# Kernel tuning notes

Hardware: AMD Instinct MI355X
Metric: run time of the kernel (lower is better)

The kernel has to match this reference:

```python
import jax, jax.numpy as jnp
import numpy as np
from jax import lax

B, S, C_IN, D, H, P, W, DFF, K = 32, 4096, 32, 256, 8, 24, 64, 512, 5
DH = D // H
EPS = 1e-5


def _make_starts():
    stride = max(1, W // 2)
    idx = list(range(0, max(S - W + 1, 1), stride))
    if len(idx) == 0 or idx[-1] != S - W:
        if S - W >= 0:
            idx.append(S - W)
    return np.asarray(idx)

STARTS = _make_starts()                      # [M]
WIDX = STARTS[:, None] + np.arange(W)        # [M, W] patch gather indices


def setup_inputs() -> dict:
    key = jax.random.key(0)
    ks = jax.random.split(key, 24)
    r = lambda i, shape, s=0.02: (jax.random.normal(ks[i], shape, jnp.float32) * s)
    return {
        "x": jax.random.normal(ks[0], (B, S, C_IN), jnp.float32),
        "last_close_unused": jnp.zeros((B,), jnp.float32),
        "dw_w": r(1, (C_IN, 1, K), 0.2),      # depthwise conv kernel
        "pw_w": r(2, (D, C_IN), 0.1),         # pointwise conv (1x1)
        "bn_g": jnp.ones((D,), jnp.float32),
        "bn_b": jnp.zeros((D,), jnp.float32),
        "lg_Wq": r(3, (D, D)), "lg_Wk": r(4, (D, D)),
        "lg_Wv": r(5, (D, D)), "lg_Wo": r(6, (D, D)),
        "dec_Qd": r(7, (P, D), 1.0 / np.sqrt(D)),
        "dec_Wq": r(8, (D, D)), "dec_Wk": r(9, (D, D)),
        "dec_Wv": r(10, (D, D)), "dec_Wo": r(11, (D, D)),
        "ff1_w": r(12, (DFF, D)), "ff1_b": jnp.zeros((DFF,), jnp.float32),
        "ff2_w": r(13, (D, DFF)), "ff2_b": jnp.zeros((D,), jnp.float32),
        "out_w": r(14, (1, D)), "out_b": jnp.zeros((1,), jnp.float32),
        "gate_logits": jnp.tile(jnp.array([0.2, 0.4, 0.4], jnp.float32), (P, 1)),
    }


def _ln(x):
    m = x.mean(-1, keepdims=True)
    v = ((x - m) ** 2).mean(-1, keepdims=True)
    return (x - m) / jnp.sqrt(v + EPS)


def _split(t):  # [B, L, D] -> [B, H, L, DH]
    return t.reshape(t.shape[0], -1, H, DH).transpose(0, 2, 1, 3)


def _mha(Q, KV, Wq, Wk, Wv, scale):
    q = _split(Q @ Wq.T)
    k = _split(KV @ Wk.T)
    v = _split(KV @ Wv.T)
    attn = jax.nn.softmax(jnp.einsum('bhqd,bhkd->bhqk', q, k) * scale, axis=-1)
    o = jnp.einsum('bhqk,bhkd->bhqd', attn, v)
    o = o.transpose(0, 2, 1, 3).reshape(Q.shape[0], -1, D)
    return o, attn


def reference(x, last_close_unused, dw_w, pw_w, bn_g, bn_b,
              lg_Wq, lg_Wk, lg_Wv, lg_Wo,
              dec_Qd, dec_Wq, dec_Wk, dec_Wv, dec_Wo,
              ff1_w, ff1_b, ff2_w, ff2_b, out_w, out_b, gate_logits):
    # --- DepthwisePointwise front-end ---
    xt = jnp.transpose(x, (0, 2, 1))                         # [B, C, S]
    z = lax.conv_general_dilated(xt, dw_w, (1,), [(K // 2, K // 2)],
                                 dimension_numbers=('NCH', 'OIH', 'NCH'),
                                 feature_group_count=C_IN)
    z = jnp.einsum('dc,bcs->bds', pw_w, z)                   # pointwise 1x1
    z = jax.nn.gelu(z, approximate=False)
    m = z.mean((0, 2), keepdims=True)                        # BatchNorm1d (batch stats)
    v = ((z - m) ** 2).mean((0, 2), keepdims=True)
    z = (z - m) / jnp.sqrt(v + EPS) * bn_g[None, :, None] + bn_b[None, :, None]
    z = jnp.transpose(z, (0, 2, 1))                          # [B, S, D]

    # --- LocalGlobalAttention: patch-mean queries over full sequence K/V ---
    Q = z[:, WIDX].mean(axis=2)                              # [B, M, D]
    scale = 1.0 / np.sqrt(DH)
    o, attn_g = _mha(Q, z, lg_Wq, lg_Wk, lg_Wv, scale)
    Hh = _ln(o @ lg_Wo.T + Q)                                # [B, M, D]

    # --- CrossDecoder: learned queries ---
    Qd = jnp.broadcast_to(dec_Qd[None], (B, P, D))
    o2, attn_d = _mha(Qd, Hh, dec_Wq, dec_Wk, dec_Wv, scale)
    z2 = _ln(o2 @ dec_Wo.T + Qd)
    u = jax.nn.gelu(z2 @ ff1_w.T + ff1_b, approximate=False)
    u = _ln(u @ ff2_w.T + ff2_b + z2)
    y_global = (u @ out_w.T + out_b)[..., 0]                 # [B, P]

    # --- Gated combine: residual=0, local=global ---
    g = jax.nn.softmax(gate_logits, axis=-1)                 # [P, 3]
    y = g[:, 1][None, :] * y_global + g[:, 2][None, :] * y_global
    return (y, attn_g, attn_d)
```

## Files before the change

### kernel.cpp

```cpp
#include <hip/hip_runtime.h>
#include <hip/hip_bf16.h>
#include <cmath>

typedef unsigned short u16;
typedef __attribute__((ext_vector_type(4))) float f32x4;
typedef __attribute__((ext_vector_type(8))) short s16x8;

__device__ __forceinline__ float b2f(u16 u) { return __uint_as_float(((unsigned)u) << 16); }
__device__ __forceinline__ u16 f2b(float f) {
    unsigned u = __float_as_uint(f);
    unsigned r = (u + 0x7fffu + ((u >> 16) & 1u)) >> 16;
    return (u16)r;
}
__device__ __forceinline__ float gelu_f(float x) {
    float t = x * (0.7978845608f + 0.0356774081f * x * x);
    float e = exp2f(2.885390082f * t);
    return 0.5f * x * (1.0f + (e - 1.0f) / (e + 1.0f));
}

#define FOLD 0.25503590f

__global__ __launch_bounds__(256) void prep0_k(const float* __restrict__ pw_w,
        const float* __restrict__ lg_Wq, const float* __restrict__ lg_Wo,
        const float* __restrict__ dec_Wk, const float* __restrict__ dec_Wv,
        const float* __restrict__ dec_Wo, const float* __restrict__ ff1_w,
        const float* __restrict__ ff2_w,
        u16* __restrict__ pwb, u16* __restrict__ Wq_b, u16* __restrict__ Wo_b,
        u16* __restrict__ Wk2_b, u16* __restrict__ Wv2_b, u16* __restrict__ Wo2b,
        u16* __restrict__ ff1b, u16* __restrict__ ff2b)
{
    int idx = blockIdx.x * 256 + threadIdx.x;
    if (idx < 327680) {
        int which = idx >> 16, r = idx & 65535;
        const float* srcs[5] = {lg_Wq, lg_Wo, dec_Wk, dec_Wv, dec_Wo};
        u16* dsts[5] = {Wq_b, Wo_b, Wk2_b, Wv2_b, Wo2b};
        dsts[which][r] = f2b(srcs[which][r]);
    } else if (idx < 458752) {
        int r = idx - 327680;
        ff1b[r] = f2b(ff1_w[r]);
    } else if (idx < 589824) {
        int r = idx - 458752;
        ff2b[r] = f2b(ff2_w[r]);
    } else {
        int r = idx - 589824;
        pwb[r] = f2b(pw_w[r]);
    }
}

__global__ __launch_bounds__(256) void dwpw_k(const float* __restrict__ x,
        const float* __restrict__ dw_w, const u16* __restrict__ pwb,
        u16* __restrict__ zp, float* __restrict__ csum, float* __restrict__ csum2)
{
    __shared__ float xs[68][33];
    __shared__ __align__(16) u16 As[64][40];
    const int t = threadIdx.x;
    const int b = blockIdx.x >> 6, s0 = (blockIdx.x & 63) << 6;
    const int r0 = blockIdx.x * 64;
    const int lane = t & 63, w = t >> 6;
    const int l16 = lane & 15, hi = lane >> 4;

    for (int idx = t; idx < 68 * 32; idx += 256) {
        int row = idx >> 5, c = idx & 31;
        int sg = s0 - 2 + row;
        xs[row][c] = (sg >= 0 && sg < 4096) ? x[((size_t)b * 4096 + sg) * 32 + c] : 0.0f;
    }
    const int cc = t & 31;
    float wv[5];
    #pragma unroll
    for (int k = 0; k < 5; ++k) wv[k] = dw_w[cc * 5 + k];
    __syncthreads();
    #pragma unroll
    for (int i = 0; i < 8; ++i) {
        int sl = (t + i * 256) >> 5;
        float acc = 0;
        #pragma unroll
        for (int k = 0; k < 5; ++k) acc += xs[sl + k][cc] * wv[k];
        As[sl][cc] = f2b(acc);
    }
    __syncthreads();

    const int n0 = w * 64;
    f32x4 zero = {0, 0, 0, 0};
    s16x8 bf[4];
    #pragma unroll
    for (int ni = 0; ni < 4; ++ni)
        bf[ni] = *(const s16x8*)(pwb + (n0 + ni * 16 + l16) * 32 + hi * 8);

    float cl[4] = {0,0,0,0}, ch[4] = {0,0,0,0};
    float ql[4] = {0,0,0,0}, qh[4] = {0,0,0,0};

    #pragma unroll
    for (int mi = 0; mi < 4; ++mi) {
        s16x8 af = *(const s16x8*)&As[mi * 16 + l16][hi * 8];
        #pragma unroll
        for (int ni = 0; ni < 4; ++ni) {
            f32x4 acc = __builtin_amdgcn_mfma_f32_16x16x32_bf16(af, bf[ni], zero, 0, 0, 0);
            int col = n0 + ni * 16 + l16;
            int rowb = r0 + mi * 16 + hi * 4;
            #pragma unroll
            for (int r = 0; r < 4; ++r) {
                float e = gelu_f(acc[r]);
                zp[(size_t)(rowb + r) * 256 + col] = f2b(e);
                if (mi < 2) { cl[ni] += e; ql[ni] += e * e; }
                else        { ch[ni] += e; qh[ni] += e * e; }
            }
        }
    }
    #pragma unroll
    for (int ni = 0; ni < 4; ++ni) {
        #pragma unroll
        for (int m = 16; m <= 32; m <<= 1) {
            cl[ni] += __shfl_xor(cl[ni], m);
            ch[ni] += __shfl_xor(ch[ni], m);
            ql[ni] += __shfl_xor(ql[ni], m);
            qh[ni] += __shfl_xor(qh[ni], m);
        }
        if (lane < 16) {
            int col = n0 + ni * 16 + lane;
            size_t bc = (size_t)(r0 >> 5);
            csum [bc * 256 + col]       = cl[ni];
            csum [(bc + 1) * 256 + col] = ch[ni];
            csum2[bc * 256 + col]       = ql[ni];
            csum2[(bc + 1) * 256 + col] = qh[ni];
        }
    }
}

__global__ __launch_bounds__(256) void stats2_k(const float* __restrict__ csum,
        const float* __restrict__ csum2, float* __restrict__ statp)
{
    int j = blockIdx.x, t = threadIdx.x;
    float s1 = 0, s2 = 0;
    for (int i = 0; i < 64; ++i) {
        s1 += csum [(size_t)(j * 64 + i) * 256 + t];
        s2 += csum2[(size_t)(j * 64 + i) * 256 + t];
    }
    statp[j * 512 + t] = s1;
    statp[j * 512 + 256 + t] = s2;
}

__global__ __launch_bounds__(256) void prep1_k(const float* __restrict__ statp,
        const float* __restrict__ bn_g, const float* __restrict__ bn_b,
        const float* __restrict__ gate_logits,
        float* __restrict__ a_ws, float* __restrict__ c_ws, float* __restrict__ coef)
{
    int t = threadIdx.x;
    float s1 = 0, s2 = 0;
    for (int j = 0; j < 64; ++j) {
        s1 += statp[j * 512 + t];
        s2 += statp[j * 512 + 256 + t];
    }
    const float invN = 1.0f / 131072.0f;
    float mean = s1 * invN;
    float var = s2 * invN - mean * mean;
    float av = bn_g[t] * rsqrtf(var + 1e-5f);
    a_ws[t] = av;
    c_ws[t] = bn_b[t] - mean * av;
    if (t < 24) {
        float g0 = gate_logits[t * 3], g1 = gate_logits[t * 3 + 1], g2 = gate_logits[t * 3 + 2];
        float mx = fmaxf(g0, fmaxf(g1, g2));
        float e0 = __expf(g0 - mx), e1 = __expf(g1 - mx), e2 = __expf(g2 - mx);
        coef[t] = (e1 + e2) / (e0 + e1 + e2);
    }
}

__global__ __launch_bounds__(256) void prepx_k(const float* __restrict__ lg_Wk,
        const float* __restrict__ lg_Wv, const float* __restrict__ a_ws,
        const float* __restrict__ c_ws, const float* __restrict__ dec_Qd,
        const float* __restrict__ dec_Wq, const float* __restrict__ csum,
        const u16* __restrict__ Wq_b,
        u16* __restrict__ Wk_b, u16* __restrict__ Wv_b,
        float* __restrict__ betak, float* __restrict__ betav,
        float* __restrict__ q2, u16* __restrict__ qb)
{
    __shared__ __align__(16) char sm[41728];
    const int bid = blockIdx.x, t = threadIdx.x;
    if (bid < 512) {
        float* red = (float*)sm;
        int which = bid >> 8, row = bid & 255;
        const float* Wsrc = which ? lg_Wv : lg_Wk;
        float wv = Wsrc[row * 256 + t];
        (which ? Wv_b : Wk_b)[row * 256 + t] = f2b(wv * a_ws[t]);
        float v = wv * c_ws[t];
        for (int m = 32; m; m >>= 1) v += __shfl_xor(v, m);
        if ((t & 63) == 0) red[t >> 6] = v;
        __syncthreads();
        if (t == 0) (which ? betav : betak)[row] = red[0] + red[1] + red[2] + red[3];
    } else if (bid < 528) {
        float (*wq)[260] = (float(*)[260])sm;
        float (*qd)[260] = (float(*)[260])(sm + 16640);
        int j = bid - 512;
        for (int idx = t; idx < 4096; idx += 256) {
            int tl = idx >> 8, d = idx & 255;
            wq[tl][d] = dec_Wq[(j * 16 + tl) * 256 + d];
        }
        for (int idx = t; idx < 6144; idx += 256) {
            int p = idx >> 8, d = idx & 255;
            qd[p][d] = dec_Qd[idx];
        }
        __syncthreads();
        for (int o = t; o < 384; o += 256) {
            int p = o >> 4, tl = o & 15;
            float s = 0;
            #pragma unroll 8
            for (int d = 0; d < 256; ++d) s += qd[p][d] * wq[tl][d];
            q2[p * 256 + j * 16 + tl] = s;
        }
    } else {
        u16* As = (u16*)sm;
        float* aa = (float*)(sm + 32768);
        float* ccx = (float*)(sm + 33792);
        const int r0 = (bid - 528) * 64;
        const int lane = t & 63, w = t >> 6;
        const int l16 = lane & 15, hi = lane >> 4;
        aa[t] = a_ws[t] * 0.015625f;
        ccx[t] = c_ws[t];
        __syncthreads();
        #pragma unroll
        for (int i = 0; i < 8; ++i) {
            int c = t + i * 256;
            int row = c >> 5, c16 = c & 31;
            int g = r0 + row, mm = g & 127;
            u16 tmp[8];
            if (mm == 127) {
                #pragma unroll
                for (int j = 0; j < 8; ++j) tmp[j] = 0;
            } else {
                const float* c0p = csum + (size_t)g * 256 + c16 * 8;
                const float* c1p = c0p + 256;
                #pragma unroll
                for (int j = 0; j < 8; ++j) {
                    int d = c16 * 8 + j;
                    tmp[j] = f2b((c0p[j] + c1p[j]) * aa[d] + ccx[d]);
                }
            }
            int boff = (c16 * 16) ^ ((row & 7) << 4);
            *(s16x8*)((char*)As + row * 512 + boff) = *(s16x8*)tmp;
        }
        __syncthreads();
        const int n0 = w * 64;
        f32x4 zero = {0, 0, 0, 0};
        f32x4 acc[4][4];
        #pragma unroll
        for (int mi = 0; mi < 4; ++mi)
            #pragma unroll
            for (int ni = 0; ni < 4; ++ni) acc[mi][ni] = zero;
        #pragma unroll
        for (int kk = 0; kk < 8; ++kk) {
            s16x8 af[4], bf[4];
            #pragma unroll
            for (int mi = 0; mi < 4; ++mi) {
                int row = mi * 16 + l16;
                int boff = (kk * 64 + hi * 16) ^ ((row & 7) << 4);
                af[mi] = *(const s16x8*)((const char*)As + row * 512 + boff);
            }
            #pragma unroll
            for (int ni = 0; ni < 4; ++ni)
                bf[ni] = *(const s16x8*)(Wq_b + (n0 + ni * 16 + l16) * 256 + kk * 32 + hi * 8);
            #pragma unroll
            for (int mi = 0; mi < 4; ++mi)
                #pragma unroll
                for (int ni = 0; ni < 4; ++ni)
                    acc[mi][ni] = __builtin_amdgcn_mfma_f32_16x16x32_bf16(af[mi], bf[ni], acc[mi][ni], 0, 0, 0);
        }
        #pragma unroll
        for (int mi = 0; mi < 4; ++mi)
            #pragma unroll
            for (int ni = 0; ni < 4; ++ni) {
                int col = n0 + ni * 16 + l16;
                int rowb = r0 + mi * 16 + hi * 4;
                #pragma unroll
                for (int r = 0; r < 4; ++r)
                    qb[(size_t)(rowb + r) * 256 + col] = f2b(acc[mi][ni][r] * FOLD);
            }
    }
}

__global__ __launch_bounds__(256) void kv_k(const u16* __restrict__ zp,
        const u16* __restrict__ Wk, const u16* __restrict__ Wv,
        const float* __restrict__ betak, const float* __restrict__ betav,
        u16* __restrict__ kb, u16* __restrict__ vT)
{
    __shared__ __align__(16) char smem[36864];
    const int t = threadIdx.x;
    const int r0 = blockIdx.x * 64;
    const int lane = t & 63, w = t >> 6;
    const int l16 = lane & 15, hi = lane >> 4;

    const u16* Ag = zp + (size_t)r0 * 256;
    #pragma unroll
    for (int i = 0; i < 8; ++i) {
        int c = t + i * 256;
        int row = c >> 5, c16 = c & 31;
        s16x8 v = *(const s16x8*)(Ag + row * 256 + c16 * 8);
        int boff = (c16 * 16) ^ ((row & 7) << 4);
        *(s16x8*)(smem + row * 512 + boff) = v;
    }
    __syncthreads();

    const int n0 = w * 64;
    f32x4 zero = {0, 0, 0, 0};
    f32x4 acc[4][4];
    #pragma unroll
    for (int mi = 0; mi < 4; ++mi)
        #pragma unroll
        for (int ni = 0; ni < 4; ++ni) acc[mi][ni] = zero;

    #pragma unroll
    for (int kk = 0; kk < 8; ++kk) {
        s16x8 af[4], bfk[4];
        #pragma unroll
        for (int mi = 0; mi < 4; ++mi) {
            int row = mi * 16 + l16;
            int boff = (kk * 64 + hi * 16) ^ ((row & 7) << 4);
            af[mi] = *(const s16x8*)(smem + row * 512 + boff);
        }
        #pragma unroll
        for (int ni = 0; ni < 4; ++ni)
            bfk[ni] = *(const s16x8*)(Wk + (n0 + ni * 16 + l16) * 256 + kk * 32 + hi * 8);
        #pragma unroll
        for (int mi = 0; mi < 4; ++mi)
            #pragma unroll
            for (int ni = 0; ni < 4; ++ni)
                acc[mi][ni] = __builtin_amdgcn_mfma_f32_16x16x32_bf16(af[mi], bfk[ni], acc[mi][ni], 0, 0, 0);
    }
    #pragma unroll
    for (int mi = 0; mi < 4; ++mi)
        #pragma unroll
        for (int ni = 0; ni < 4; ++ni) {
            int col = n0 + ni * 16 + l16;
            float bv = betak[col];
            int rowb = r0 + mi * 16 + hi * 4;
            #pragma unroll
            for (int r = 0; r < 4; ++r)
                kb[(size_t)(rowb + r) * 256 + col] = f2b(acc[mi][ni][r] + bv);
        }

    #pragma unroll
    for (int mi = 0; mi < 4; ++mi)
        #pragma unroll
        for (int ni = 0; ni < 4; ++ni) acc[mi][ni] = zero;
    #pragma unroll
    for (int kk = 0; kk < 8; ++kk) {
        s16x8 af[4], bfv[4];
        #pragma unroll
        for (int mi = 0; mi < 4; ++mi) {
            int row = mi * 16 + l16;
            int boff = (kk * 64 + hi * 16) ^ ((row & 7) << 4);
            af[mi] = *(const s16x8*)(smem + row * 512 + boff);
        }
        #pragma unroll
        for (int ni = 0; ni < 4; ++ni)
            bfv[ni] = *(const s16x8*)(Wv + (n0 + ni * 16 + l16) * 256 + kk * 32 + hi * 8);
        #pragma unroll
        for (int mi = 0; mi < 4; ++mi)
            #pragma unroll
            for (int ni = 0; ni < 4; ++ni)
                acc[mi][ni] = __builtin_amdgcn_mfma_f32_16x16x32_bf16(af[mi], bfv[ni], acc[mi][ni], 0, 0, 0);
    }
    __syncthreads();
    #pragma unroll
    for (int mi = 0; mi < 4; ++mi)
        #pragma unroll
        for (int ni = 0; ni < 4; ++ni) {
            int col = n0 + ni * 16 + l16;
            float bv = betav[col];
            int rowb = mi * 16 + hi * 4;
            ushort4 pk;
            pk.x = f2b(acc[mi][ni][0] + bv);
            pk.y = f2b(acc[mi][ni][1] + bv);
            pk.z = f2b(acc[mi][ni][2] + bv);
            pk.w = f2b(acc[mi][ni][3] + bv);
            char* p = smem + col * 144 + ((((rowb >> 3) ^ (col & 7)) & 7) << 4) + ((rowb & 7) << 1);
            *(ushort4*)p = pk;
        }
    __syncthreads();
    const int b = r0 >> 12;
    const int sblk = (r0 & 4095) >> 6;
    u16* vout = vT + (size_t)(b * 8) * 131072 + (size_t)sblk * 2048;
    #pragma unroll
    for (int j = 0; j < 8; ++j) {
        int gid = j * 256 + t;
        int col = gid >> 3, oct = gid & 7;
        const char* p = smem + col * 144 + (((oct ^ (col & 7)) & 7) << 4);
        s16x8 v = *(const s16x8*)p;
        int h = col >> 5, dh = col & 31;
        *(s16x8*)(vout + (size_t)h * 131072 + dh * 64 + oct * 8) = v;
    }
}

template<int MODE>
__global__ __launch_bounds__(256) void gemm_g(const u16* __restrict__ A,
        const u16* __restrict__ W, const float* __restrict__ bias,
        void* __restrict__ Cout, int K, int ntn)
{
    __shared__ u16 As[64 * 256];
    const int t = threadIdx.x;
    const int rt = blockIdx.x / ntn, nt = blockIdx.x % ntn;
    const int r0 = rt * 64, N = ntn * 256;
    const int lane = t & 63, w = t >> 6;
    const int l16 = lane & 15, hi = lane >> 4;

    const u16* Ag = A + (size_t)r0 * K;
    const int n0 = w * 64;
    f32x4 zero = {0, 0, 0, 0};
    f32x4 acc[4][4];
    #pragma unroll
    for (int mi = 0; mi < 4; ++mi)
        #pragma unroll
        for (int ni = 0; ni < 4; ++ni) acc[mi][ni] = zero;

    for (int kc = 0; kc < K; kc += 256) {
        if (kc) __syncthreads();
        #pragma unroll
        for (int i = 0; i < 8; ++i) {
            int c = t + i * 256;
            int row = c >> 5, c16 = c & 31;
            s16x8 v = *(const s16x8*)(Ag + (size_t)row * K + kc + c16 * 8);
            int boff = (c16 * 16) ^ ((row & 7) << 4);
            *(s16x8*)((char*)As + row * 512 + boff) = v;
        }
        __syncthreads();
        #pragma unroll
        for (int kk = 0; kk < 8; ++kk) {
            s16x8 af[4], bf[4];
            #pragma unroll
            for (int mi = 0; mi < 4; ++mi) {
                int row = mi * 16 + l16;
                int boff = (kk * 64 + hi * 16) ^ ((row & 7) << 4);
                af[mi] = *(const s16x8*)((const char*)As + row * 512 + boff);
            }
            #pragma unroll
            for (int ni = 0; ni < 4; ++ni) {
                int j = nt * 256 + n0 + ni * 16 + l16;
                bf[ni] = *(const s16x8*)(W + (size_t)j * K + kc + kk * 32 + hi * 8);
            }
            #pragma unroll
            for (int mi = 0; mi < 4; ++mi)
                #pragma unroll
                for (int ni = 0; ni < 4; ++ni)
                    acc[mi][ni] = __builtin_amdgcn_mfma_f32_16x16x32_bf16(af[mi], bf[ni], acc[mi][ni], 0, 0, 0);
        }
    }

    #pragma unroll
    for (int mi = 0; mi < 4; ++mi)
        #pragma unroll
        for (int ni = 0; ni < 4; ++ni) {
            int col = nt * 256 + n0 + ni * 16 + l16;
            float bv = bias ? bias[col] : 0.0f;
            int rowb = r0 + mi * 16 + hi * 4;
            #pragma unroll
            for (int r = 0; r < 4; ++r) {
                float v = acc[mi][ni][r] + bv;
                if (MODE == 0)      ((u16*)Cout)[(size_t)(rowb + r) * N + col] = f2b(v);
                else if (MODE == 1) ((float*)Cout)[(size_t)(rowb + r) * N + col] = v;
                else                ((u16*)Cout)[(size_t)(rowb + r) * N + col] = f2b(gelu_f(v));
            }
        }
}

__global__ __launch_bounds__(256) void gemm_dual(const u16* __restrict__ A,
        const u16* __restrict__ W0, const u16* __restrict__ W1,
        u16* __restrict__ C0, u16* __restrict__ C1)
{
    __shared__ u16 As[64 * 256];
    const int t = threadIdx.x;
    const int which = blockIdx.x >> 6;
    const int r0 = (blockIdx.x & 63) * 64;
    const u16* W = which ? W1 : W0;
    u16* C = which ? C1 : C0;
    const int lane = t & 63, w = t >> 6;
    const int l16 = lane & 15, hi = lane >> 4;

    const u16* Ag = A + (size_t)r0 * 256;
    #pragma unroll
    for (int i = 0; i < 8; ++i) {
        int c = t + i * 256;
        int row = c >> 5, c16 = c & 31;
        s16x8 v = *(const s16x8*)(Ag + row * 256 + c16 * 8);
        int boff = (c16 * 16) ^ ((row & 7) << 4);
        *(s16x8*)((char*)As + row * 512 + boff) = v;
    }
    __syncthreads();

    const int n0 = w * 64;
    f32x4 zero = {0, 0, 0, 0};
    f32x4 acc[4][4];
    #pragma unroll
    for (int mi = 0; mi < 4; ++mi)
        #pragma unroll
        for (int ni = 0; ni < 4; ++ni) acc[mi][ni] = zero;

    #pragma unroll
    for (int kk = 0; kk < 8; ++kk) {
        s16x8 af[4], bf[4];
        #pragma unroll
        for (int mi = 0; mi < 4; ++mi) {
            int row = mi * 16 + l16;
            int boff = (kk * 64 + hi * 16) ^ ((row & 7) << 4);
            af[mi] = *(const s16x8*)((const char*)As + row * 512 + boff);
        }
        #pragma unroll
        for (int ni = 0; ni < 4; ++ni)
            bf[ni] = *(const s16x8*)(W + (n0 + ni * 16 + l16) * 256 + kk * 32 + hi * 8);
        #pragma unroll
        for (int mi = 0; mi < 4; ++mi)
            #pragma unroll
            for (int ni = 0; ni < 4; ++ni)
                acc[mi][ni] = __builtin_amdgcn_mfma_f32_16x16x32_bf16(af[mi], bf[ni], acc[mi][ni], 0, 0, 0);
    }
    #pragma unroll
    for (int mi = 0; mi < 4; ++mi)
        #pragma unroll
        for (int ni = 0; ni < 4; ++ni) {
            int col = n0 + ni * 16 + l16;
            int rowb = r0 + mi * 16 + hi * 4;
            #pragma unroll
            for (int r = 0; r < 4; ++r)
                C[(size_t)(rowb + r) * 256 + col] = f2b(acc[mi][ni][r]);
        }
}

__global__ __launch_bounds__(512) void attn_p1(const u16* __restrict__ qb,
        const u16* __restrict__ kb, const u16* __restrict__ vT,
        float* __restrict__ den, float* __restrict__ o_part)
{
    const int bid = blockIdx.x;
    const int b = bid >> 6, h = (bid >> 3) & 7, chunk = bid & 7;
    const int t = threadIdx.x, w = t >> 6, lane = t & 63;
    const int l16 = lane & 15, hi = lane >> 4;

    __shared__ u16 p_lds[8][16][48];

    s16x8 qf = *(const s16x8*)(qb + ((size_t)(b * 128 + w * 16 + l16)) * 256 + h * 32 + hi * 8);
    const u16* kbase = kb + (size_t)b * 4096 * 256 + h * 32 + hi * 8;
    const u16* vbase = vT + (size_t)(b * 8 + h) * 131072 + hi * 8;

    float dacc[4] = {0, 0, 0, 0};
    f32x4 zero = {0, 0, 0, 0};
    f32x4 oacc[2]; oacc[0] = zero; oacc[1] = zero;

    const int sbeg = chunk * 512, send = sbeg + 512;
    s16x8 kf0 = *(const s16x8*)(kbase + (size_t)(sbeg + l16) * 256);
    s16x8 kf1 = *(const s16x8*)(kbase + (size_t)(sbeg + 16 + l16) * 256);
    s16x8 vf0 = *(const s16x8*)(vbase + (sbeg >> 6) * 2048 + l16 * 64 + (sbeg & 63));
    s16x8 vf1 = *(const s16x8*)(vbase + (sbeg >> 6) * 2048 + (16 + l16) * 64 + (sbeg & 63));

    for (int s0 = sbeg; s0 < send; s0 += 32) {
        s16x8 k0 = kf0, k1 = kf1, v0 = vf0, v1 = vf1;
        int sn = s0 + 32;
        if (sn < send) {
            kf0 = *(const s16x8*)(kbase + (size_t)(sn + l16) * 256);
            kf1 = *(const s16x8*)(kbase + (size_t)(sn + 16 + l16) * 256);
            vf0 = *(const s16x8*)(vbase + (sn >> 6) * 2048 + l16 * 64 + (sn & 63));
            vf1 = *(const s16x8*)(vbase + (sn >> 6) * 2048 + (16 + l16) * 64 + (sn & 63));
        }
        f32x4 lg0 = __builtin_amdgcn_mfma_f32_16x16x32_bf16(qf, k0, zero, 0, 0, 0);
        f32x4 lg1 = __builtin_amdgcn_mfma_f32_16x16x32_bf16(qf, k1, zero, 0, 0, 0);
        #pragma unroll
        for (int r = 0; r < 4; ++r) {
            float e0 = exp2f(lg0[r]);
            float e1 = exp2f(lg1[r]);
            dacc[r] += e0 + e1;
            p_lds[w][hi * 4 + r][l16] = f2b(e0);
            p_lds[w][hi * 4 + r][16 + l16] = f2b(e1);
        }
        s16x8 pf = *(const s16x8*)(&p_lds[w][l16][hi * 8]);
        oacc[0] = __builtin_amdgcn_mfma_f32_16x16x32_bf16(pf, v0, oacc[0], 0, 0, 0);
        oacc[1] = __builtin_amdgcn_mfma_f32_16x16x32_bf16(pf, v1, oacc[1], 0, 0, 0);
    }

    #pragma unroll
    for (int m = 1; m <= 8; m <<= 1) {
        #pragma unroll
        for (int r = 0; r < 4; ++r) dacc[r] += __shfl_xor(dacc[r], m);
    }
    if (l16 == 0) {
        #pragma unroll
        for (int r = 0; r < 4; ++r)
            den[(size_t)chunk * 32768 + (b * 8 + h) * 128 + w * 16 + hi * 4 + r] = dacc[r];
    }
    #pragma unroll
    for (int vi = 0; vi < 2; ++vi)
        #pragma unroll
        for (int r = 0; r < 4; ++r) {
            int mg = w * 16 + hi * 4 + r;
            o_part[(size_t)chunk * 1048576 + (size_t)(b * 128 + mg) * 256 + h * 32 + vi * 16 + l16] = oacc[vi][r];
        }
}

__global__ __launch_bounds__(256) void norm_k(const float* __restrict__ o_part,
        const float* __restrict__ den, u16* __restrict__ ob)
{
    int idx4 = blockIdx.x * 256 + threadIdx.x;
    int row = idx4 >> 6;
    int col4 = (idx4 & 63) * 4;
    int b = row >> 7, m = row & 127, h = col4 >> 5;
    f32x4 s = {0, 0, 0, 0};
    #pragma unroll
    for (int c = 0; c < 8; ++c)
        s += *(const f32x4*)(o_part + (size_t)c * 1048576 + (size_t)row * 256 + col4);
    float ds = 0;
    int di = (b * 8 + h) * 128 + m;
    #pragma unroll
    for (int c = 0; c < 8; ++c) ds += den[(size_t)c * 32768 + di];
    float rinv = 1.0f / ds;
    ushort4 o;
    o.x = f2b(s[0] * rinv); o.y = f2b(s[1] * rinv);
    o.z = f2b(s[2] * rinv); o.w = f2b(s[3] * rinv);
    *(ushort4*)(ob + (size_t)row * 256 + col4) = o;
}

__global__ __launch_bounds__(512) void attn_p2(const u16* __restrict__ qb,
        const u16* __restrict__ kb, const float* __restrict__ den,
        float* __restrict__ attn_out)
{
    const int bid = blockIdx.x;
    const int b = bid >> 6, h = (bid >> 3) & 7, chunk = bid & 7;
    const int t = threadIdx.x, w = t >> 6, lane = t & 63;
    const int l16 = lane & 15, hi = lane >> 4;

    __shared__ float buf[8][16][68];

    s16x8 qf = *(const s16x8*)(qb + ((size_t)(b * 128 + w * 16 + l16)) * 256 + h * 32 + hi * 8);
    const u16* kbase = kb + (size_t)b * 4096 * 256 + h * 32 + hi * 8;

    float rinv[4];
    #pragma unroll
    for (int r = 0; r < 4; ++r) {
        int di = (b * 8 + h) * 128 + w * 16 + hi * 4 + r;
        float ds = 0;
        #pragma unroll
        for (int c = 0; c < 8; ++c) ds += den[(size_t)c * 32768 + di];
        rinv[r] = 1.0f / ds;
    }

    f32x4 zero = {0, 0, 0, 0};
    float* ab = attn_out + (size_t)(b * 8 + h) * 127 * 4096;
    const int srow = lane >> 4;
    const int scol = (lane & 15) * 4;

    const int sbeg = chunk * 512, send = sbeg + 512;
    for (int s0 = sbeg; s0 < send; s0 += 64) {
        #pragma unroll
        for (int kk = 0; kk < 4; ++kk) {
            int sg = s0 + kk * 16 + l16;
            s16x8 kf = *(const s16x8*)(kbase + (size_t)sg * 256);
            f32x4 lg = __builtin_amdgcn_mfma_f32_16x16x32_bf16(qf, kf, zero, 0, 0, 0);
            #pragma unroll
            for (int r = 0; r < 4; ++r)
                buf[w][hi * 4 + r][kk * 16 + l16] = exp2f(lg[r]) * rinv[r];
        }
        #pragma unroll
        for (int rb = 0; rb < 4; ++rb) {
            int row = rb * 4 + srow;
            int mg = w * 16 + row;
            f32x4 v = *(const f32x4*)&buf[w][row][scol];
            if (mg < 127)
                *(f32x4*)(ab + (size_t)mg * 4096 + s0 + scol) = v;
        }
    }
}

__global__ __launch_bounds__(256) void gemm_lnhh(const u16* __restrict__ A,
        const u16* __restrict__ W, const float* __restrict__ csum,
        const float* __restrict__ a_ws, const float* __restrict__ c_ws,
        u16* __restrict__ Hb)
{
    __shared__ __align__(16) char sm[67584];
    __shared__ float aa[256], cc2[256];
    u16* As = (u16*)sm;
    float (*Cs)[264] = (float(*)[264])sm;
    const int t = threadIdx.x;
    const int r0 = blockIdx.x * 64;
    const int lane = t & 63, w = t >> 6;
    const int l16 = lane & 15, hi = lane >> 4;

    aa[t] = a_ws[t] * 0.015625f;
    cc2[t] = c_ws[t];

    const u16* Ag = A + (size_t)r0 * 256;
    #pragma unroll
    for (int i = 0; i < 8; ++i) {
        int c = t + i * 256;
        int row = c >> 5, c16 = c & 31;
        s16x8 v = *(const s16x8*)(Ag + row * 256 + c16 * 8);
        int boff = (c16 * 16) ^ ((row & 7) << 4);
        *(s16x8*)(sm + row * 512 + boff) = v;
    }
    __syncthreads();

    const int n0 = w * 64;
    f32x4 zero = {0, 0, 0, 0};
    f32x4 acc[4][4];
    #pragma unroll
    for (int mi = 0; mi < 4; ++mi)
        #pragma unroll
        for (int ni = 0; ni < 4; ++ni) acc[mi][ni] = zero;
    #pragma unroll
    for (int kk = 0; kk < 8; ++kk) {
        s16x8 af[4], bf[4];
        #pragma unroll
        for (int mi = 0; mi < 4; ++mi) {
            int row = mi * 16 + l16;
            int boff = (kk * 64 + hi * 16) ^ ((row & 7) << 4);
            af[mi] = *(const s16x8*)(sm + row * 512 + boff);
        }
        #pragma unroll
        for (int ni = 0; ni < 4; ++ni)
            bf[ni] = *(const s16x8*)(W + (n0 + ni * 16 + l16) * 256 + kk * 32 + hi * 8);
        #pragma unroll
        for (int mi = 0; mi < 4; ++mi)
            #pragma unroll
            for (int ni = 0; ni < 4; ++ni)
                acc[mi][ni] = __builtin_amdgcn_mfma_f32_16x16x32_bf16(af[mi], bf[ni], acc[mi][ni], 0, 0, 0);
    }
    __syncthreads();
    #pragma unroll
    for (int mi = 0; mi < 4; ++mi)
        #pragma unroll
        for (int ni = 0; ni < 4; ++ni) {
            int col = n0 + ni * 16 + l16;
            int rowb = mi * 16 + hi * 4;
            #pragma unroll
            for (int r = 0; r < 4; ++r)
                Cs[rowb + r][col] = acc[mi][ni][r];
        }
    __syncthreads();
    for (int pass = 0; pass < 16; ++pass) {
        int row = pass * 4 + w;
        int g = r0 + row, mm = g & 127;
        float v[4];
        #pragma unroll
        for (int j = 0; j < 4; ++j) {
            int d = lane + j * 64;
            float qv = 0.0f;
            if (mm != 127)
                qv = (csum[(size_t)g * 256 + d] + csum[(size_t)(g + 1) * 256 + d]) * aa[d] + cc2[d];
            v[j] = Cs[row][d] + qv;
        }
        float s = v[0] + v[1] + v[2] + v[3];
        for (int m = 32; m; m >>= 1) s += __shfl_xor(s, m);
        float mean = s * (1.0f / 256.0f);
        float q = 0;
        #pragma unroll
        for (int j = 0; j < 4; ++j) { float d_ = v[j] - mean; q += d_ * d_; }
        for (int m = 32; m; m >>= 1) q += __shfl_xor(q, m);
        float rs = rsqrtf(q * (1.0f / 256.0f) + 1e-5f);
        #pragma unroll
        for (int j = 0; j < 4; ++j)
            Hb[(size_t)g * 256 + lane + j * 64] = f2b((v[j] - mean) * rs);
    }
}

__global__ __launch_bounds__(256) void dec_attn_k(const float* __restrict__ q2,
        const u16* __restrict__ k2b, const u16* __restrict__ v2b,
        float* __restrict__ attn_d, u16* __restrict__ o2b)
{
    __shared__ float qs2[24 * 32];
    __shared__ float ks[128][33];
    __shared__ float vs[128][33];
    __shared__ float lg2[24 * 128];
    __shared__ float sinv[24];
    int bid = blockIdx.x, b = bid >> 3, h = bid & 7;
    int t = threadIdx.x;
    const float scale = 0.17677669529663687f;
    for (int idx = t; idx < 4096; idx += 256) {
        int row = idx >> 5, c = idx & 31;
        ks[row][c] = b2f(k2b[((size_t)(b * 128 + row)) * 256 + h * 32 + c]);
        vs[row][c] = b2f(v2b[((size_t)(b * 128 + row)) * 256 + h * 32 + c]);
    }
    for (int idx = t; idx < 768; idx += 256) {
        int p = idx >> 5, i = idx & 31;
        qs2[idx] = q2[p * 256 + h * 32 + i];
    }
    __syncthreads();
    for (int idx = t; idx < 3048; idx += 256) {
        int p = idx / 127, m = idx - p * 127;
        float s = 0;
        #pragma unroll 8
        for (int i = 0; i < 32; ++i) s += qs2[p * 32 + i] * ks[m][i];
        lg2[p * 128 + m] = __expf(s * scale);
    }
    __syncthreads();
    if (t < 24) {
        float s = 0;
        for (int m = 0; m < 127; ++m) s += lg2[t * 128 + m];
        sinv[t] = 1.0f / s;
    }
    __syncthreads();
    float* ad = attn_d + (size_t)bid * 24 * 127;
    for (int idx = t; idx < 3048; idx += 256) {
        int p = idx / 127, m = idx - p * 127;
        float av = lg2[p * 128 + m] * sinv[p];
        lg2[p * 128 + m] = av;
        ad[idx] = av;
    }
    __syncthreads();
    for (int idx = t; idx < 768; idx += 256) {
        int p = idx >> 5, dh = idx & 31;
        float s = 0;
        for (int m = 0; m < 127; ++m)
            s += lg2[p * 128 + m] * vs[m][dh];
        o2b[((size_t)(b * 24 + p)) * 256 + h * 32 + dh] = f2b(s);
    }
}

__global__ __launch_bounds__(256) void gemm_ln3(const u16* __restrict__ A,
        const u16* __restrict__ W, const float* __restrict__ dec_Qd,
        float* __restrict__ z2f, u16* __restrict__ z2b)
{
    __shared__ __align__(16) char sm[67584];
    u16* As = (u16*)sm;
    float (*Cs)[264] = (float(*)[264])sm;
    const int t = threadIdx.x;
    const int r0 = blockIdx.x * 64;
    const int lane = t & 63, w = t >> 6;
    const int l16 = lane & 15, hi = lane >> 4;

    const u16* Ag = A + (size_t)r0 * 256;
    #pragma unroll
    for (int i = 0; i < 8; ++i) {
        int c = t + i * 256;
        int row = c >> 5, c16 = c & 31;
        s16x8 v = *(const s16x8*)(Ag + row * 256 + c16 * 8);
        int boff = (c16 * 16) ^ ((row & 7) << 4);
        *(s16x8*)(sm + row * 512 + boff) = v;
    }
    __syncthreads();

    const int n0 = w * 64;
    f32x4 zero = {0, 0, 0, 0};
    f32x4 acc[4][4];
    #pragma unroll
    for (int mi = 0; mi < 4; ++mi)
        #pragma unroll
        for (int ni = 0; ni < 4; ++ni) acc[mi][ni] = zero;
    #pragma unroll
    for (int kk = 0; kk < 8; ++kk) {
        s16x8 af[4], bf[4];
        #pragma unroll
        for (int mi = 0; mi < 4; ++mi) {
            int row = mi * 16 + l16;
            int boff = (kk * 64 + hi * 16) ^ ((row & 7) << 4);
            af[mi] = *(const s16x8*)(sm + row * 512 + boff);
        }
        #pragma unroll
        for (int ni = 0; ni < 4; ++ni)
            bf[ni] = *(const s16x8*)(W + (n0 + ni * 16 + l16) * 256 + kk * 32 + hi * 8);
        #pragma unroll
        for (int mi = 0; mi < 4; ++mi)
            #pragma unroll
            for (int ni = 0; ni < 4; ++ni)
                acc[mi][ni] = __builtin_amdgcn_mfma_f32_16x16x32_bf16(af[mi], bf[ni], acc[mi][ni], 0, 0, 0);
    }
    __syncthreads();
    #pragma unroll
    for (int mi = 0; mi < 4; ++mi)
        #pragma unroll
        for (int ni = 0; ni < 4; ++ni) {
            int col = n0 + ni * 16 + l16;
            int rowb = mi * 16 + hi * 4;
            #pragma unroll
            for (int r = 0; r < 4; ++r)
                Cs[rowb + r][col] = acc[mi][ni][r];
        }
    __syncthreads();
    for (int pass = 0; pass < 16; ++pass) {
        int row = pass * 4 + w;
        int g = r0 + row, p = g % 24;
        float v[4];
        #pragma unroll
        for (int j = 0; j < 4; ++j) {
            int d = lane + j * 64;
            v[j] = Cs[row][d] + dec_Qd[p * 256 + d];
        }
        float s = v[0] + v[1] + v[2] + v[3];
        for (int m = 32; m; m >>= 1) s += __shfl_xor(s, m);
        float mean = s * (1.0f / 256.0f);
        float q = 0;
        #pragma unroll
        for (int j = 0; j < 4; ++j) { float d_ = v[j] - mean; q += d_ * d_; }
        for (int m = 32; m; m >>= 1) q += __shfl_xor(q, m);
        float rs = rsqrtf(q * (1.0f / 256.0f) + 1e-5f);
        #pragma unroll
        for (int j = 0; j < 4; ++j) {
            float u = (v[j] - mean) * rs;
            z2f[(size_t)g * 256 + lane + j * 64] = u;
            z2b[(size_t)g * 256 + lane + j * 64] = f2b(u);
        }
    }
}

__global__ __launch_bounds__(256) void gemm_ln5(const u16* __restrict__ A,
        const u16* __restrict__ W, const float* __restrict__ bias,
        const float* __restrict__ z2f, const float* __restrict__ out_w,
        const float* __restrict__ out_b, const float* __restrict__ coef,
        float* __restrict__ y)
{
    __shared__ __align__(16) char sm[67584];
    u16* As = (u16*)sm;
    float (*Cs)[264] = (float(*)[264])sm;
    const int t = threadIdx.x;
    const int r0 = blockIdx.x * 64;
    const int lane = t & 63, w = t >> 6;
    const int l16 = lane & 15, hi = lane >> 4;
    const int K = 512;

    const u16* Ag = A + (size_t)r0 * K;
    const int n0 = w * 64;
    f32x4 zero = {0, 0, 0, 0};
    f32x4 acc[4][4];
    #pragma unroll
    for (int mi = 0; mi < 4; ++mi)
        #pragma unroll
        for (int ni = 0; ni < 4; ++ni) acc[mi][ni] = zero;

    for (int kc = 0; kc < K; kc += 256) {
        if (kc) __syncthreads();
        #pragma unroll
        for (int i = 0; i < 8; ++i) {
            int c = t + i * 256;
            int row = c >> 5, c16 = c & 31;
            s16x8 v = *(const s16x8*)(Ag + (size_t)row * K + kc + c16 * 8);
            int boff = (c16 * 16) ^ ((row & 7) << 4);
            *(s16x8*)(sm + row * 512 + boff) = v;
        }
        __syncthreads();
        #pragma unroll
        for (int kk = 0; kk < 8; ++kk) {
            s16x8 af[4], bf[4];
            #pragma unroll
            for (int mi = 0; mi < 4; ++mi) {
                int row = mi * 16 + l16;
                int boff = (kk * 64 + hi * 16) ^ ((row & 7) << 4);
                af[mi] = *(const s16x8*)(sm + row * 512 + boff);
            }
            #pragma unroll
            for (int ni = 0; ni < 4; ++ni)
                bf[ni] = *(const s16x8*)(W + (size_t)(n0 + ni * 16 + l16) * K + kc + kk * 32 + hi * 8);
            #pragma unroll
            for (int mi = 0; mi < 4; ++mi)
                #pragma unroll
                for (int ni = 0; ni < 4; ++ni)
                    acc[mi][ni] = __builtin_amdgcn_mfma_f32_16x16x32_bf16(af[mi], bf[ni], acc[mi][ni], 0, 0, 0);
        }
    }
    __syncthreads();
    #pragma unroll
    for (int mi = 0; mi < 4; ++mi)
        #pragma unroll
        for (int ni = 0; ni < 4; ++ni) {
            int col = n0 + ni * 16 + l16;
            int rowb = mi * 16 + hi * 4;
            #pragma unroll
            for (int r = 0; r < 4; ++r)
                Cs[rowb + r][col] = acc[mi][ni][r];
        }
    __syncthreads();
    for (int pass = 0; pass < 16; ++pass) {
        int row = pass * 4 + w;
        int g = r0 + row, p = g % 24;
        float v[4];
        #pragma unroll
        for (int j = 0; j < 4; ++j) {
            int d = lane + j * 64;
            v[j] = Cs[row][d] + bias[d] + z2f[(size_t)g * 256 + d];
        }
        float s = v[0] + v[1] + v[2] + v[3];
        for (int m = 32; m; m >>= 1) s += __shfl_xor(s, m);
        float mean = s * (1.0f / 256.0f);
        float q = 0;
        #pragma unroll
        for (int j = 0; j < 4; ++j) { float d_ = v[j] - mean; q += d_ * d_; }
        for (int m = 32; m; m >>= 1) q += __shfl_xor(q, m);
        float rs = rsqrtf(q * (1.0f / 256.0f) + 1e-5f);
        float yp = 0;
        #pragma unroll
        for (int j = 0; j < 4; ++j)
            yp += (v[j] - mean) * rs * out_w[lane + j * 64];
        for (int m = 32; m; m >>= 1) yp += __shfl_xor(yp, m);
        if (lane == 0)
            y[g] = coef[p] * (yp + out_b[0]);
    }
}

extern "C" void kernel_launch(void* const* d_in, const int* in_sizes, int n_in,
                              void* d_out, int out_size, void* d_ws, size_t ws_size,
                              hipStream_t stream)
{
    const float* x        = (const float*)d_in[0];
    const float* dw_w     = (const float*)d_in[2];
    const float* pw_w     = (const float*)d_in[3];
    const float* bn_g     = (const float*)d_in[4];
    const float* bn_b     = (const float*)d_in[5];
    const float* lg_Wq    = (const float*)d_in[6];
    const float* lg_Wk    = (const float*)d_in[7];
    const float* lg_Wv    = (const float*)d_in[8];
    const float* lg_Wo    = (const float*)d_in[9];
    const float* dec_Qd   = (const float*)d_in[10];
    const float* dec_Wq   = (const float*)d_in[11];
    const float* dec_Wk   = (const float*)d_in[12];
    const float* dec_Wv   = (const float*)d_in[13];
    const float* dec_Wo   = (const float*)d_in[14];
    const float* ff1_w    = (const float*)d_in[15];
    const float* ff1_b    = (const float*)d_in[16];
    const float* ff2_w    = (const float*)d_in[17];
    const float* ff2_b    = (const float*)d_in[18];
    const float* out_w    = (const float*)d_in[19];
    const float* out_b    = (const float*)d_in[20];
    const float* gate_lg  = (const float*)d_in[21];

    char* ws = (char*)d_ws;
    size_t off = 0;
    auto alloc = [&](size_t bytes) -> void* {
        void* p = ws + off;
        off = (off + bytes + 255) & ~(size_t)255;
        return p;
    };
    u16*   zp    = (u16*)  alloc(67108864);
    u16*   kb    = (u16*)  alloc(67108864);
    u16*   vT    = (u16*)  alloc(67108864);
    float* csum  = (float*)alloc(4194304);
    float* csum2 = (float*)alloc(4194304);
    u16*   qb    = (u16*)  alloc(2097152);
    u16*   ob    = (u16*)  alloc(2097152);
    u16*   Hb    = (u16*)  alloc(2097152);
    u16*   k2b   = (u16*)  alloc(2097152);
    u16*   v2b   = (u16*)  alloc(2097152);
    float* o_part= (float*)alloc(33554432);
    u16*   o2b   = (u16*)  alloc(393216);
    float* z2f   = (float*)alloc(786432);
    u16*   z2b   = (u16*)  alloc(393216);
    u16*   u1b   = (u16*)  alloc(786432);
    float* q2    = (float*)alloc(24576);
    float* den   = (float*)alloc(1048576);
    float* statp = (float*)alloc(131072);
    float* a_ws  = (float*)alloc(1024);
    float* c_ws  = (float*)alloc(1024);
    float* betak = (float*)alloc(1024);
    float* betav = (float*)alloc(1024);
    float* coef  = (float*)alloc(256);
    u16*   pwb   = (u16*)  alloc(16384);
    u16*   Wk_b  = (u16*)  alloc(131072);
    u16*   Wv_b  = (u16*)  alloc(131072);
    u16*   Wq_b  = (u16*)  alloc(131072);
    u16*   Wo_b  = (u16*)  alloc(131072);
    u16*   Wk2_b = (u16*)  alloc(131072);
    u16*   Wv2_b = (u16*)  alloc(131072);
    u16*   Wo2b  = (u16*)  alloc(131072);
    u16*   ff1b  = (u16*)  alloc(262144);
    u16*   ff2b  = (u16*)  alloc(262144);

    float* y_out  = (float*)d_out;
    float* attn_g = y_out + 768;
    float* attn_d = attn_g + (size_t)32 * 8 * 127 * 4096;

    prep0_k<<<2336, 256, 0, stream>>>(pw_w, lg_Wq, lg_Wo, dec_Wk, dec_Wv, dec_Wo, ff1_w, ff2_w,
                                      pwb, Wq_b, Wo_b, Wk2_b, Wv2_b, Wo2b, ff1b, ff2b);
    dwpw_k<<<2048, 256, 0, stream>>>(x, dw_w, pwb, zp, csum, csum2);
    stats2_k<<<64, 256, 0, stream>>>(csum, csum2, statp);
    prep1_k<<<1, 256, 0, stream>>>(statp, bn_g, bn_b, gate_lg, a_ws, c_ws, coef);
    prepx_k<<<592, 256, 0, stream>>>(lg_Wk, lg_Wv, a_ws, c_ws, dec_Qd, dec_Wq, csum, Wq_b,
                                     Wk_b, Wv_b, betak, betav, q2, qb);
    kv_k<<<2048, 256, 0, stream>>>(zp, Wk_b, Wv_b, betak, betav, kb, vT);
    attn_p1<<<2048, 512, 0, stream>>>(qb, kb, vT, den, o_part);
    norm_k<<<1024, 256, 0, stream>>>(o_part, den, ob);
    attn_p2<<<2048, 512, 0, stream>>>(qb, kb, den, attn_g);
    gemm_lnhh<<<64, 256, 0, stream>>>(ob, Wo_b, csum, a_ws, c_ws, Hb);
    gemm_dual<<<128, 256, 0, stream>>>(Hb, Wk2_b, Wv2_b, k2b, v2b);
    dec_attn_k<<<256, 256, 0, stream>>>(q2, k2b, v2b, attn_d, o2b);
    gemm_ln3<<<12, 256, 0, stream>>>(o2b, Wo2b, dec_Qd, z2f, z2b);
    gemm_g<2><<<24, 256, 0, stream>>>(z2b, ff1b, ff1_b, u1b, 256, 2);
    gemm_ln5<<<12, 256, 0, stream>>>(u1b, ff2b, ff2_b, z2f, out_w, out_b, coef, y_out);
}
```

Measured before the change: 601.2 us.

## Fuse attention pass 1, normalization and pass 2 into one full-sequence kernel

Merges the three global-attention kernels (chunked softmax-numerator pass, partial-sum normalization, and probability write pass) into a single kernel. Each block now handles one (batch, head) over the whole 4096-long sequence, so the denominator stays in registers and the partial output buffers are no longer written and read back. This also drops two launches. In exchange the grid shrinks from 2048 to 256 blocks, roughly one block per CU. Each block then runs two serial passes over K, which lowers available parallelism for the large attention-probability write.

```diff
diff --git a/kernel.cpp b/kernel.cpp
--- a/kernel.cpp
+++ b/kernel.cpp
@@ -522,16 +522,16 @@
         }
 }
 
-__global__ __launch_bounds__(512) void attn_p1(const u16* __restrict__ qb,
+__global__ __launch_bounds__(512) void attn_k(const u16* __restrict__ qb,
         const u16* __restrict__ kb, const u16* __restrict__ vT,
-        float* __restrict__ den, float* __restrict__ o_part)
-{
-    const int bid = blockIdx.x;
-    const int b = bid >> 6, h = (bid >> 3) & 7, chunk = bid & 7;
+        u16* __restrict__ ob, float* __restrict__ attn_out)
+{
+    const int b = blockIdx.x >> 3, h = blockIdx.x & 7;
     const int t = threadIdx.x, w = t >> 6, lane = t & 63;
     const int l16 = lane & 15, hi = lane >> 4;
 
     __shared__ u16 p_lds[8][16][48];
+    __shared__ float buf[8][16][68];
 
     s16x8 qf = *(const s16x8*)(qb + ((size_t)(b * 128 + w * 16 + l16)) * 256 + h * 32 + hi * 8);
     const u16* kbase = kb + (size_t)b * 4096 * 256 + h * 32 + hi * 8;
@@ -541,16 +541,15 @@
     f32x4 zero = {0, 0, 0, 0};
     f32x4 oacc[2]; oacc[0] = zero; oacc[1] = zero;
 
-    const int sbeg = chunk * 512, send = sbeg + 512;
-    s16x8 kf0 = *(const s16x8*)(kbase + (size_t)(sbeg + l16) * 256);
-    s16x8 kf1 = *(const s16x8*)(kbase + (size_t)(sbeg + 16 + l16) * 256);
-    s16x8 vf0 = *(const s16x8*)(vbase + (sbeg >> 6) * 2048 + l16 * 64 + (sbeg & 63));
-    s16x8 vf1 = *(const s16x8*)(vbase + (sbeg >> 6) * 2048 + (16 + l16) * 64 + (sbeg & 63));
-
-    for (int s0 = sbeg; s0 < send; s0 += 32) {
+    s16x8 kf0 = *(const s16x8*)(kbase + (size_t)l16 * 256);
+    s16x8 kf1 = *(const s16x8*)(kbase + (size_t)(16 + l16) * 256);
+    s16x8 vf0 = *(const s16x8*)(vbase + l16 * 64);
+    s16x8 vf1 = *(const s16x8*)(vbase + (16 + l16) * 64);
+
+    for (int s0 = 0; s0 < 4096; s0 += 32) {
         s16x8 k0 = kf0, k1 = kf1, v0 = vf0, v1 = vf1;
         int sn = s0 + 32;
-        if (sn < send) {
+        if (sn < 4096) {
             kf0 = *(const s16x8*)(kbase + (size_t)(sn + l16) * 256);
             kf1 = *(const s16x8*)(kbase + (size_t)(sn + 16 + l16) * 256);
             vf0 = *(const s16x8*)(vbase + (sn >> 6) * 2048 + l16 * 64 + (sn & 63));
@@ -576,73 +575,23 @@
         #pragma unroll
         for (int r = 0; r < 4; ++r) dacc[r] += __shfl_xor(dacc[r], m);
     }
-    if (l16 == 0) {
-        #pragma unroll
-        for (int r = 0; r < 4; ++r)
-            den[(size_t)chunk * 32768 + (b * 8 + h) * 128 + w * 16 + hi * 4 + r] = dacc[r];
-    }
+    float rinv[4];
+    #pragma unroll
+    for (int r = 0; r < 4; ++r) rinv[r] = 1.0f / dacc[r];
+
     #pragma unroll
     for (int vi = 0; vi < 2; ++vi)
         #pragma unroll
         for (int r = 0; r < 4; ++r) {
             int mg = w * 16 + hi * 4 + r;
-            o_part[(size_t)chunk * 1048576 + (size_t)(b * 128 + mg) * 256 + h * 32 + vi * 16 + l16] = oacc[vi][r];
-        }
-}
-
-__global__ __launch_bounds__(256) void norm_k(const float* __restrict__ o_part,
-        const float* __restrict__ den, u16* __restrict__ ob)
-{
-    int idx4 = blockIdx.x * 256 + threadIdx.x;
-    int row = idx4 >> 6;
-    int col4 = (idx4 & 63) * 4;
-    int b = row >> 7, m = row & 127, h = col4 >> 5;
-    f32x4 s = {0, 0, 0, 0};
-    #pragma unroll
-    for (int c = 0; c < 8; ++c)
-        s += *(const f32x4*)(o_part + (size_t)c * 1048576 + (size_t)row * 256 + col4);
-    float ds = 0;
-    int di = (b * 8 + h) * 128 + m;
-    #pragma unroll
-    for (int c = 0; c < 8; ++c) ds += den[(size_t)c * 32768 + di];
-    float rinv = 1.0f / ds;
-    ushort4 o;
-    o.x = f2b(s[0] * rinv); o.y = f2b(s[1] * rinv);
-    o.z = f2b(s[2] * rinv); o.w = f2b(s[3] * rinv);
-    *(ushort4*)(ob + (size_t)row * 256 + col4) = o;
-}
-
-__global__ __launch_bounds__(512) void attn_p2(const u16* __restrict__ qb,
-        const u16* __restrict__ kb, const float* __restrict__ den,
-        float* __restrict__ attn_out)
-{
-    const int bid = blockIdx.x;
-    const int b = bid >> 6, h = (bid >> 3) & 7, chunk = bid & 7;
-    const int t = threadIdx.x, w = t >> 6, lane = t & 63;
-    const int l16 = lane & 15, hi = lane >> 4;
-
-    __shared__ float buf[8][16][68];
-
-    s16x8 qf = *(const s16x8*)(qb + ((size_t)(b * 128 + w * 16 + l16)) * 256 + h * 32 + hi * 8);
-    const u16* kbase = kb + (size_t)b * 4096 * 256 + h * 32 + hi * 8;
-
-    float rinv[4];
-    #pragma unroll
-    for (int r = 0; r < 4; ++r) {
-        int di = (b * 8 + h) * 128 + w * 16 + hi * 4 + r;
-        float ds = 0;
-        #pragma unroll
-        for (int c = 0; c < 8; ++c) ds += den[(size_t)c * 32768 + di];
-        rinv[r] = 1.0f / ds;
-    }
-
-    f32x4 zero = {0, 0, 0, 0};
+            ob[(size_t)(b * 128 + mg) * 256 + h * 32 + vi * 16 + l16] = f2b(oacc[vi][r] * rinv[r]);
+        }
+
     float* ab = attn_out + (size_t)(b * 8 + h) * 127 * 4096;
     const int srow = lane >> 4;
     const int scol = (lane & 15) * 4;
 
-    const int sbeg = chunk * 512, send = sbeg + 512;
-    for (int s0 = sbeg; s0 < send; s0 += 64) {
+    for (int s0 = 0; s0 < 4096; s0 += 64) {
         #pragma unroll
         for (int kk = 0; kk < 4; ++kk) {
             int sg = s0 + kk * 16 + l16;
@@ -670,7 +619,6 @@
 {
     __shared__ __align__(16) char sm[67584];
     __shared__ float aa[256], cc2[256];
-    u16* As = (u16*)sm;
     float (*Cs)[264] = (float(*)[264])sm;
     const int t = threadIdx.x;
     const int r0 = blockIdx.x * 64;
@@ -812,7 +760,6 @@
         float* __restrict__ z2f, u16* __restrict__ z2b)
 {
     __shared__ __align__(16) char sm[67584];
-    u16* As = (u16*)sm;
     float (*Cs)[264] = (float(*)[264])sm;
     const int t = threadIdx.x;
     const int r0 = blockIdx.x * 64;
@@ -900,7 +847,6 @@
         float* __restrict__ y)
 {
     __shared__ __align__(16) char sm[67584];
-    u16* As = (u16*)sm;
     float (*Cs)[264] = (float(*)[264])sm;
     const int t = threadIdx.x;
     const int r0 = blockIdx.x * 64;
@@ -1029,13 +975,11 @@
     u16*   Hb    = (u16*)  alloc(2097152);
     u16*   k2b   = (u16*)  alloc(2097152);
     u16*   v2b   = (u16*)  alloc(2097152);
-    float* o_part= (float*)alloc(33554432);
     u16*   o2b   = (u16*)  alloc(393216);
     float* z2f   = (float*)alloc(786432);
     u16*   z2b   = (u16*)  alloc(393216);
     u16*   u1b   = (u16*)  alloc(786432);
     float* q2    = (float*)alloc(24576);
-    float* den   = (float*)alloc(1048576);
     float* statp = (float*)alloc(131072);
     float* a_ws  = (float*)alloc(1024);
     float* c_ws  = (float*)alloc(1024);
@@ -1065,9 +1009,7 @@
     prepx_k<<<592, 256, 0, stream>>>(lg_Wk, lg_Wv, a_ws, c_ws, dec_Qd, dec_Wq, csum, Wq_b,
                                      Wk_b, Wv_b, betak, betav, q2, qb);
     kv_k<<<2048, 256, 0, stream>>>(zp, Wk_b, Wv_b, betak, betav, kb, vT);
-    attn_p1<<<2048, 512, 0, stream>>>(qb, kb, vT, den, o_part);
-    norm_k<<<1024, 256, 0, stream>>>(o_part, den, ob);
-    attn_p2<<<2048, 512, 0, stream>>>(qb, kb, den, attn_g);
+    attn_k<<<256, 512, 0, stream>>>(qb, kb, vT, ob, attn_g);
     gemm_lnhh<<<64, 256, 0, stream>>>(ob, Wo_b, csum, a_ws, c_ws, Hb);
     gemm_dual<<<128, 256, 0, stream>>>(Hb, Wk2_b, Wv2_b, k2b, v2b);
     dec_attn_k<<<256, 256, 0, stream>>>(q2, k2b, v2b, attn_d, o2b);
```

After: 579.9 us. 1.04x faster.
